# Optimization experiments

Hardware: AMD Instinct MI355X
Metric: run time of the kernel (lower is better)

The kernel has to match this reference:

```python
import jax, jax.numpy as jnp
import numpy as np

B, S, D, E, H, SL = 4, 2048, 2048, 16, 1024, 1
NUM_SLOTS = E * SL
TEMP = 1.0
TOP_K = 2
EPS = 1e-8


def setup_inputs() -> dict:
    key = jax.random.key(0)
    k0, k1, k2, k3 = jax.random.split(key, 4)
    x = jax.random.normal(k0, (B, S, D), dtype=jnp.float32)
    Wd = jax.random.normal(k1, (NUM_SLOTS, D), dtype=jnp.float32) * 0.02
    W1 = jax.random.normal(k2, (E, D, H), dtype=jnp.float32) * 0.02
    b1 = jnp.zeros((E, H), dtype=jnp.float32)
    W2 = jax.random.normal(k3, (E, H, D), dtype=jnp.float32) * 0.02
    b2 = jnp.zeros((E, D), dtype=jnp.float32)
    return {"x": x, "Wd": Wd, "W1": W1, "b1": b1, "W2": W2, "b2": b2}


def reference(x, Wd, W1, b1, W2, b2):
    lead = x.shape[:-1]
    xf = x.reshape(-1, D)                      # [T, D]
    T = xf.shape[0]

    logits = (xf @ Wd.T) / TEMP                # [T, num_slots]
    dispatch = jax.nn.softmax(logits, axis=0)  # softmax over tokens
    combine = jax.nn.softmax(logits, axis=-1)  # softmax over slots

    # Aggregate tokens into slots, run all experts as one batched GEMM chain.
    slot_in = (dispatch.T @ xf).reshape(E, SL, D)                    # [E, SL, D]
    h = jax.nn.gelu(jnp.einsum('esd,edh->esh', slot_in, W1) + b1[:, None, :],
                    approximate=False)
    slot_out = (jnp.einsum('esh,ehd->esd', h, W2) + b2[:, None, :]).reshape(NUM_SLOTS, D)

    out = (combine @ slot_out).reshape(x.shape)

    # Router stats / losses (eval mode: no EMA update of train_scores).
    expert_weights = combine.reshape(T, E, SL).mean(-1)              # [T, E]
    mean_usage = expert_weights.mean(0)                              # [E]
    p = jax.nn.softmax(Wd.mean(0).reshape(E, -1).mean(-1))
    router_loss = E * jnp.sum(mean_usage * p)

    topk_w, topk_idx = jax.lax.top_k(expert_weights, TOP_K)
    topk_w_norm = topk_w / jnp.clip(topk_w.sum(-1, keepdims=True), EPS)

    gate_weights = expert_weights.reshape(*lead, E)
    routing_entropy = -(gate_weights * jnp.log(gate_weights + EPS)).sum(-1).mean()

    return (out,
            router_loss,
            gate_weights,
            topk_idx.reshape(*lead, TOP_K),
            topk_w_norm.reshape(*lead, TOP_K),
            mean_usage,
            routing_entropy,
            dispatch.reshape(*lead, NUM_SLOTS))
```

## Files before the change

kernel.cpp:

```cpp
#include <hip/hip_runtime.h>
#include <math.h>

#define TTOK 8192
#define DIM  2048
#define NEXP 16
#define NH   1024

#define OFF_PART1   0u
#define OFF_LOGITS  2097152u
#define OFF_COMBINE 2228224u
#define OFF_NUM     2359296u
#define OFF_PART6   2490368u
#define OFF_RAWH    4587520u
#define OFF_PART10  4849664u
#define OFF_SLOTOUT 5373952u
#define OFF_CMAX    5406720u
#define OFF_CSUM    5407232u
#define OFF_MUSUM   5407744u
#define OFF_ENT     5408256u
#define OFF_M       5408288u
#define OFF_INVS    5408304u

#define O_OUT   0u
#define O_LOSS  16777216u
#define O_GATE  16777217u
#define O_TOPI  16908289u
#define O_TOPW  16924673u
#define O_MU    16941057u
#define O_ENTR  16941073u
#define O_DISP  16941074u

__device__ __forceinline__ float wave_sum(float v){
  #pragma unroll
  for (int o=1;o<64;o<<=1) v += __shfl_xor(v,o,64);
  return v;
}
__device__ __forceinline__ float wave_max(float v){
  #pragma unroll
  for (int o=1;o<64;o<<=1) v = fmaxf(v,__shfl_xor(v,o,64));
  return v;
}

__global__ __launch_bounds__(256) void k1_logits(const float* __restrict__ x,
                                                 const float* __restrict__ Wd,
                                                 float* __restrict__ part1){
  const int tb = blockIdx.x >> 4;
  const int kc = blockIdx.x & 15;
  const int t  = tb*256 + threadIdx.x;
  const float4* __restrict__ xr = (const float4*)(x + (size_t)t*DIM + kc*128);
  float acc[16];
  #pragma unroll
  for (int e=0;e<16;e++) acc[e]=0.f;
  #pragma unroll 4
  for (int k4=0;k4<32;k4++){
    float4 xv = xr[k4];
    #pragma unroll
    for (int e=0;e<16;e++){
      float4 w = *(const float4*)(Wd + e*DIM + kc*128 + k4*4);
      acc[e] += xv.x*w.x + xv.y*w.y + xv.z*w.z + xv.w*w.w;
    }
  }
  float4* po = (float4*)(part1 + ((size_t)kc*TTOK + t)*16);
  po[0] = make_float4(acc[0],acc[1],acc[2],acc[3]);
  po[1] = make_float4(acc[4],acc[5],acc[6],acc[7]);
  po[2] = make_float4(acc[8],acc[9],acc[10],acc[11]);
  po[3] = make_float4(acc[12],acc[13],acc[14],acc[15]);
}

__global__ __launch_bounds__(256) void k2_row(const float* __restrict__ part1,
    float* __restrict__ logits, float* __restrict__ combine,
    float* __restrict__ gate_out, float* __restrict__ topi_out, float* __restrict__ topw_out,
    float* __restrict__ colmax_part, float* __restrict__ musum_part, float* __restrict__ ent_part){
  const int tid = threadIdx.x;
  const int t = blockIdx.x*256 + tid;
  float l[16];
  #pragma unroll
  for (int e=0;e<16;e++) l[e]=0.f;
  for (int kc=0;kc<16;kc++){
    const float4* pr = (const float4*)(part1 + ((size_t)kc*TTOK + t)*16);
    #pragma unroll
    for (int q=0;q<4;q++){
      float4 v = pr[q];
      l[q*4+0]+=v.x; l[q*4+1]+=v.y; l[q*4+2]+=v.z; l[q*4+3]+=v.w;
    }
  }
  float4* lo = (float4*)(logits + (size_t)t*16);
  lo[0]=make_float4(l[0],l[1],l[2],l[3]);   lo[1]=make_float4(l[4],l[5],l[6],l[7]);
  lo[2]=make_float4(l[8],l[9],l[10],l[11]); lo[3]=make_float4(l[12],l[13],l[14],l[15]);
  float m = l[0];
  #pragma unroll
  for (int e=1;e<16;e++) m = fmaxf(m,l[e]);
  float c[16]; float s=0.f;
  #pragma unroll
  for (int e=0;e<16;e++){ c[e]=expf(l[e]-m); s+=c[e]; }
  float inv = 1.f/s;
  #pragma unroll
  for (int e=0;e<16;e++) c[e]*=inv;
  float4* co = (float4*)(combine + (size_t)t*16);
  co[0]=make_float4(c[0],c[1],c[2],c[3]);   co[1]=make_float4(c[4],c[5],c[6],c[7]);
  co[2]=make_float4(c[8],c[9],c[10],c[11]); co[3]=make_float4(c[12],c[13],c[14],c[15]);
  float* go = gate_out + (size_t)t*16;
  #pragma unroll
  for (int e=0;e<16;e++) go[e]=c[e];
  float v0=-1.f, v1=-1.f; int i0=0, i1=0;
  #pragma unroll
  for (int e=0;e<16;e++){
    float ce=c[e];
    if (ce>v0){ v1=v0; i1=i0; v0=ce; i0=e; }
    else if (ce>v1){ v1=ce; i1=e; }
  }
  float dn = fmaxf(v0+v1, 1e-8f);
  topi_out[(size_t)t*2+0]=(float)i0; topi_out[(size_t)t*2+1]=(float)i1;
  topw_out[(size_t)t*2+0]=v0/dn;     topw_out[(size_t)t*2+1]=v1/dn;
  float ent=0.f;
  #pragma unroll
  for (int e=0;e<16;e++) ent -= c[e]*logf(c[e]+1e-8f);

  __shared__ float red[4][16];
  __shared__ float rede[4];
  const int w = tid>>6, lane = tid&63;
  #pragma unroll
  for (int e=0;e<16;e++){ float v=wave_max(l[e]); if(lane==0) red[w][e]=v; }
  __syncthreads();
  if (tid<16){
    float v=fmaxf(fmaxf(red[0][tid],red[1][tid]),fmaxf(red[2][tid],red[3][tid]));
    colmax_part[blockIdx.x*16+tid]=v;
  }
  __syncthreads();
  #pragma unroll
  for (int e=0;e<16;e++){ float v=wave_sum(c[e]); if(lane==0) red[w][e]=v; }
  { float v=wave_sum(ent); if(lane==0) rede[w]=v; }
  __syncthreads();
  if (tid<16) musum_part[blockIdx.x*16+tid]=red[0][tid]+red[1][tid]+red[2][tid]+red[3][tid];
  if (tid==0) ent_part[blockIdx.x]=rede[0]+rede[1]+rede[2]+rede[3];
}

__global__ __launch_bounds__(256) void k3_finalize(const float* __restrict__ Wd,
    const float* __restrict__ colmax_part, const float* __restrict__ musum_part,
    const float* __restrict__ ent_part,
    float* __restrict__ m_ws, float* __restrict__ loss_out,
    float* __restrict__ mu_out, float* __restrict__ ent_out){
  const int tid = threadIdx.x;
  __shared__ float sq[16][16];
  __shared__ float smu[16];
  __shared__ float sqe[16];
  {
    int s = tid>>4, e = tid&15;
    const float* base = Wd + (size_t)s*DIM + e*128;
    float q=0.f;
    for (int i=0;i<128;i+=4){ float4 v=*(const float4*)(base+i); q+=v.x+v.y+v.z+v.w; }
    sq[s][e]=q;
  }
  if (tid<16){
    float mm=-INFINITY, mu=0.f;
    for (int b=0;b<32;b++){ mm=fmaxf(mm,colmax_part[b*16+tid]); mu+=musum_part[b*16+tid]; }
    m_ws[tid]=mm;
    mu/=8192.f;
    mu_out[tid]=mu; smu[tid]=mu;
  }
  if (tid==32){ float es=0.f; for(int b=0;b<32;b++) es+=ent_part[b]; ent_out[0]=es/8192.f; }
  __syncthreads();
  __shared__ float sqv[16];
  if (tid<16){ float q=0.f; for(int s=0;s<16;s++) q+=sq[s][tid]; sqv[tid]=q/2048.f; }
  __syncthreads();
  if (tid<16){
    float qm=-INFINITY;
    for (int e=0;e<16;e++) qm=fmaxf(qm,sqv[e]);
    sqe[tid]=expf(sqv[tid]-qm);
  }
  __syncthreads();
  if (tid==0){
    float qs=0.f; for(int e=0;e<16;e++) qs+=sqe[e];
    float loss=0.f; for(int e=0;e<16;e++) loss+=smu[e]*(sqe[e]/qs);
    loss_out[0]=16.f*loss;
  }
}

__global__ __launch_bounds__(256) void k4_num(const float* __restrict__ logits,
    const float* __restrict__ m_ws, float* __restrict__ num, float* __restrict__ colsum_part){
  const int tid=threadIdx.x;
  const int t=blockIdx.x*256+tid;
  float mm[16];
  {
    const float4* mp=(const float4*)m_ws;
    #pragma unroll
    for (int q=0;q<4;q++){ float4 v=mp[q]; mm[q*4]=v.x; mm[q*4+1]=v.y; mm[q*4+2]=v.z; mm[q*4+3]=v.w; }
  }
  const float4* lr=(const float4*)(logits+(size_t)t*16);
  float n[16];
  #pragma unroll
  for (int q=0;q<4;q++){
    float4 v=lr[q];
    n[q*4+0]=expf(v.x-mm[q*4+0]); n[q*4+1]=expf(v.y-mm[q*4+1]);
    n[q*4+2]=expf(v.z-mm[q*4+2]); n[q*4+3]=expf(v.w-mm[q*4+3]);
  }
  float4* no=(float4*)(num+(size_t)t*16);
  no[0]=make_float4(n[0],n[1],n[2],n[3]);   no[1]=make_float4(n[4],n[5],n[6],n[7]);
  no[2]=make_float4(n[8],n[9],n[10],n[11]); no[3]=make_float4(n[12],n[13],n[14],n[15]);
  __shared__ float red[4][16];
  const int w=tid>>6, lane=tid&63;
  #pragma unroll
  for (int e=0;e<16;e++){ float v=wave_sum(n[e]); if(lane==0) red[w][e]=v; }
  __syncthreads();
  if (tid<16) colsum_part[blockIdx.x*16+tid]=red[0][tid]+red[1][tid]+red[2][tid]+red[3][tid];
}

__global__ void k5_invs(const float* __restrict__ colsum_part, float* __restrict__ inv_s){
  int tid=threadIdx.x;
  if (tid<16){ float s=0.f; for(int b=0;b<32;b++) s+=colsum_part[b*16+tid]; inv_s[tid]=1.f/s; }
}

__global__ __launch_bounds__(256) void k5b_disp(const float* __restrict__ num,
    const float* __restrict__ inv_s, float* __restrict__ disp_out){
  int i = blockIdx.x*256 + threadIdx.x;
  disp_out[i] = num[i]*inv_s[i&15];
}

__global__ __launch_bounds__(256) void k6_slotin(const float* __restrict__ x,
    const float* __restrict__ num, float* __restrict__ part6){
  const int tc = blockIdx.x >> 2;
  const int dc = blockIdx.x & 3;
  const int d  = dc*512 + threadIdx.x*2;
  const int t0 = tc*128;
  float2 acc[16];
  #pragma unroll
  for (int e=0;e<16;e++){ acc[e].x=0.f; acc[e].y=0.f; }
  #pragma unroll 4
  for (int t=0;t<128;t++){
    float2 xv = *(const float2*)(x + (size_t)(t0+t)*DIM + d);
    const float* nr = num + (size_t)(t0+t)*16;
    #pragma unroll
    for (int e=0;e<16;e++){
      float nv = nr[e];
      acc[e].x = fmaf(nv,xv.x,acc[e].x);
      acc[e].y = fmaf(nv,xv.y,acc[e].y);
    }
  }
  #pragma unroll
  for (int e=0;e<16;e++)
    *(float2*)(part6 + ((size_t)tc*16+e)*DIM + d) = acc[e];
}

__global__ __launch_bounds__(256) void k8_h(const float* __restrict__ part6,
    const float* __restrict__ W1, float* __restrict__ rawh){
  const int e   = blockIdx.x >> 4;
  const int dcc = blockIdx.x & 15;
  const int dbase = dcc*128;
  const int tid = threadIdx.x;
  __shared__ float sl[128];
  if (tid<128){
    float s=0.f;
    for (int tc=0;tc<64;tc++) s += part6[((size_t)tc*16+e)*DIM + dbase + tid];
    sl[tid]=s;
  }
  __syncthreads();
  const int hq = tid*4;
  float4 acc = make_float4(0.f,0.f,0.f,0.f);
  #pragma unroll 8
  for (int d=0; d<128; d++){
    float4 w = *(const float4*)(W1 + ((size_t)e*DIM + dbase + d)*NH + hq);
    float s = sl[d];
    acc.x=fmaf(s,w.x,acc.x); acc.y=fmaf(s,w.y,acc.y);
    acc.z=fmaf(s,w.z,acc.z); acc.w=fmaf(s,w.w,acc.w);
  }
  *(float4*)(rawh + ((size_t)dcc*16+e)*NH + hq) = acc;
}

__global__ __launch_bounds__(256) void k10_so(const float* __restrict__ rawh,
    const float* __restrict__ W2, const float* __restrict__ b1,
    const float* __restrict__ inv_s, float* __restrict__ part10){
  const int e  = blockIdx.x >> 4;
  const int hc = blockIdx.x & 15;
  const int hbase = hc*64;
  const int tid = threadIdx.x;
  __shared__ float hh[64];
  if (tid<64){
    float s=0.f;
    for (int dcc=0;dcc<16;dcc++) s += rawh[((size_t)dcc*16+e)*NH + hbase + tid];
    float pre = inv_s[e]*s + b1[(size_t)e*NH + hbase + tid];
    hh[tid] = 0.5f*pre*(1.f+erff(pre*0.70710678118654752f));
  }
  __syncthreads();
  const int d0 = tid*4, d1 = (tid+256)*4;
  float4 a0=make_float4(0,0,0,0), a1=make_float4(0,0,0,0);
  #pragma unroll 4
  for (int j=0;j<64;j++){
    const float* wrow = W2 + ((size_t)e*NH + hbase + j)*DIM;
    float4 w0 = *(const float4*)(wrow + d0);
    float4 w1 = *(const float4*)(wrow + d1);
    float s = hh[j];
    a0.x=fmaf(s,w0.x,a0.x); a0.y=fmaf(s,w0.y,a0.y); a0.z=fmaf(s,w0.z,a0.z); a0.w=fmaf(s,w0.w,a0.w);
    a1.x=fmaf(s,w1.x,a1.x); a1.y=fmaf(s,w1.y,a1.y); a1.z=fmaf(s,w1.z,a1.z); a1.w=fmaf(s,w1.w,a1.w);
  }
  *(float4*)(part10 + ((size_t)hc*16+e)*DIM + d0) = a0;
  *(float4*)(part10 + ((size_t)hc*16+e)*DIM + d1) = a1;
}

__global__ __launch_bounds__(256) void k11_sofin(const float* __restrict__ part10,
    const float* __restrict__ b2, float* __restrict__ slot_out){
  int i = blockIdx.x*256 + threadIdx.x;
  float s=0.f;
  #pragma unroll
  for (int hc=0;hc<16;hc++) s += part10[(size_t)hc*32768 + i];
  slot_out[i] = s + b2[i];
}

__global__ __launch_bounds__(256) void k12_out(const float* __restrict__ slot_out,
    const float* __restrict__ combine, float* __restrict__ out){
  const int tb = blockIdx.x >> 1;
  const int dc = blockIdx.x & 1;
  const int t0 = tb*32;
  const int d  = dc*1024 + threadIdx.x*4;
  float4 sv[16];
  #pragma unroll
  for (int e=0;e<16;e++) sv[e] = *(const float4*)(slot_out + (size_t)e*DIM + d);
  for (int t=0;t<32;t++){
    const float* cr = combine + (size_t)(t0+t)*16;
    float4 a = make_float4(0,0,0,0);
    #pragma unroll
    for (int e=0;e<16;e++){
      float c = cr[e];
      a.x=fmaf(c,sv[e].x,a.x); a.y=fmaf(c,sv[e].y,a.y);
      a.z=fmaf(c,sv[e].z,a.z); a.w=fmaf(c,sv[e].w,a.w);
    }
    *(float4*)(out + (size_t)(t0+t)*DIM + d) = a;
  }
}

extern "C" void kernel_launch(void* const* d_in, const int* in_sizes, int n_in,
                              void* d_out, int out_size, void* d_ws, size_t ws_size,
                              hipStream_t stream) {
  const float* x  = (const float*)d_in[0];
  const float* Wd = (const float*)d_in[1];
  const float* W1 = (const float*)d_in[2];
  const float* b1 = (const float*)d_in[3];
  const float* W2 = (const float*)d_in[4];
  const float* b2 = (const float*)d_in[5];
  float* out = (float*)d_out;
  float* ws  = (float*)d_ws;

  float* part1   = ws + OFF_PART1;
  float* logits  = ws + OFF_LOGITS;
  float* combine = ws + OFF_COMBINE;
  float* num     = ws + OFF_NUM;
  float* part6   = ws + OFF_PART6;
  float* rawh    = ws + OFF_RAWH;
  float* part10  = ws + OFF_PART10;
  float* slot_out= ws + OFF_SLOTOUT;
  float* cmaxp   = ws + OFF_CMAX;
  float* csump   = ws + OFF_CSUM;
  float* musump  = ws + OFF_MUSUM;
  float* entp    = ws + OFF_ENT;
  float* m_ws    = ws + OFF_M;
  float* inv_s   = ws + OFF_INVS;

  float* o_out  = out + O_OUT;
  float* o_loss = out + O_LOSS;
  float* o_gate = out + O_GATE;
  float* o_topi = out + O_TOPI;
  float* o_topw = out + O_TOPW;
  float* o_mu   = out + O_MU;
  float* o_ent  = out + O_ENTR;
  float* o_disp = out + O_DISP;

  k1_logits<<<512, 256, 0, stream>>>(x, Wd, part1);
  k2_row<<<32, 256, 0, stream>>>(part1, logits, combine, o_gate, o_topi, o_topw,
                                 cmaxp, musump, entp);
  k3_finalize<<<1, 256, 0, stream>>>(Wd, cmaxp, musump, entp, m_ws, o_loss, o_mu, o_ent);
  k4_num<<<32, 256, 0, stream>>>(logits, m_ws, num, csump);
  k5_invs<<<1, 64, 0, stream>>>(csump, inv_s);
  k5b_disp<<<512, 256, 0, stream>>>(num, inv_s, o_disp);
  k6_slotin<<<256, 256, 0, stream>>>(x, num, part6);
  k8_h<<<256, 256, 0, stream>>>(part6, W1, rawh);
  k10_so<<<256, 256, 0, stream>>>(rawh, W2, b1, inv_s, part10);
  k11_sofin<<<128, 256, 0, stream>>>(part10, b2, slot_out);
  k12_out<<<512, 256, 0, stream>>>(slot_out, combine, o_out);
}
```

Measured before the change: 192.7 us.

## Drop column-max pass, split reductions into more blocks across MoE pipeline

Removes the per-column max subtraction from the token-softmax, computing exp(logits) directly and fusing the partial-logit reduction with the column-sum in a new kernel. It also re-tiles the slot aggregation, expert GEMMs and output kernels into many more smaller blocks, with separate reduction and GELU kernels. The aim is to raise occupancy on the small-grid stages and remove one kernel pass. Skipping the max subtraction risks overflow for large logits, and more partial buffers add memory traffic.

New measurement: 199.3 us. +3.4%, slower.

```diff
diff --git a/kernel.cpp b/kernel.cpp
--- a/kernel.cpp
+++ b/kernel.cpp
@@ -3,23 +3,22 @@
 
 #define TTOK 8192
 #define DIM  2048
-#define NEXP 16
 #define NH   1024
 
 #define OFF_PART1   0u
 #define OFF_LOGITS  2097152u
-#define OFF_COMBINE 2228224u
-#define OFF_NUM     2359296u
+#define OFF_NUM     2228224u
+#define OFF_COMBINE 2359296u
 #define OFF_PART6   2490368u
-#define OFF_RAWH    4587520u
-#define OFF_PART10  4849664u
-#define OFF_SLOTOUT 5373952u
-#define OFF_CMAX    5406720u
-#define OFF_CSUM    5407232u
-#define OFF_MUSUM   5407744u
-#define OFF_ENT     5408256u
-#define OFF_M       5408288u
-#define OFF_INVS    5408304u
+#define OFF_SRAW    10878976u
+#define OFF_RAWH    10911744u
+#define OFF_H       11960320u
+#define OFF_PART10  11976704u
+#define OFF_SLOTOUT 14073856u
+#define OFF_CSUM    14106624u
+#define OFF_MUSUM   14108672u
+#define OFF_ENT     14109696u
+#define OFF_INVS    14109760u
 
 #define O_OUT   0u
 #define O_LOSS  16777216u
@@ -33,11 +32,6 @@
 __device__ __forceinline__ float wave_sum(float v){
   #pragma unroll
   for (int o=1;o<64;o<<=1) v += __shfl_xor(v,o,64);
-  return v;
-}
-__device__ __forceinline__ float wave_max(float v){
-  #pragma unroll
-  for (int o=1;o<64;o<<=1) v = fmaxf(v,__shfl_xor(v,o,64));
   return v;
 }
 
@@ -67,26 +61,65 @@
   po[3] = make_float4(acc[12],acc[13],acc[14],acc[15]);
 }
 
-__global__ __launch_bounds__(256) void k2_row(const float* __restrict__ part1,
-    float* __restrict__ logits, float* __restrict__ combine,
-    float* __restrict__ gate_out, float* __restrict__ topi_out, float* __restrict__ topw_out,
-    float* __restrict__ colmax_part, float* __restrict__ musum_part, float* __restrict__ ent_part){
-  const int tid = threadIdx.x;
-  const int t = blockIdx.x*256 + tid;
+__global__ __launch_bounds__(256) void k2a_num(const float* __restrict__ part1,
+    float* __restrict__ logits, float* __restrict__ num, float* __restrict__ colsum_part){
+  const int tid = threadIdx.x;
+  const int i = blockIdx.x*256 + tid;
+  const float4* p1 = (const float4*)part1;
+  float4 s = make_float4(0,0,0,0);
+  #pragma unroll
+  for (int kc=0;kc<16;kc++){
+    float4 v = p1[(size_t)kc*32768 + i];
+    s.x+=v.x; s.y+=v.y; s.z+=v.z; s.w+=v.w;
+  }
+  ((float4*)logits)[i] = s;
+  float4 n = make_float4(expf(s.x),expf(s.y),expf(s.z),expf(s.w));
+  ((float4*)num)[i] = n;
+  #pragma unroll
+  for (int o=4;o<64;o<<=1){
+    n.x += __shfl_xor(n.x,o,64); n.y += __shfl_xor(n.y,o,64);
+    n.z += __shfl_xor(n.z,o,64); n.w += __shfl_xor(n.w,o,64);
+  }
+  __shared__ float4 red[4][4];
+  const int w = tid>>6, lane = tid&63;
+  if (lane<4) red[w][lane] = n;
+  __syncthreads();
+  if (tid<4){
+    float4 a = red[0][tid], b = red[1][tid], c = red[2][tid], d = red[3][tid];
+    float4 t = make_float4(a.x+b.x+c.x+d.x, a.y+b.y+c.y+d.y,
+                           a.z+b.z+c.z+d.z, a.w+b.w+c.w+d.w);
+    *(float4*)(colsum_part + blockIdx.x*16 + tid*4) = t;
+  }
+}
+
+__global__ __launch_bounds__(256) void k5_invs(const float* __restrict__ colsum_part,
+                                               float* __restrict__ inv_s){
+  const int tid = threadIdx.x;
+  const int e = tid&15, sl = tid>>4;
+  float s = 0.f;
+  #pragma unroll
+  for (int k=0;k<8;k++) s += colsum_part[(sl*8+k)*16 + e];
+  __shared__ float L[16][16];
+  L[sl][e] = s;
+  __syncthreads();
+  if (tid<16){
+    float v=0.f;
+    #pragma unroll
+    for (int q=0;q<16;q++) v += L[q][tid];
+    inv_s[tid] = 1.f/v;
+  }
+}
+
+__global__ __launch_bounds__(128) void k2b_row(const float* __restrict__ logits,
+    float* __restrict__ combine, float* __restrict__ gate_out,
+    float* __restrict__ topi_out, float* __restrict__ topw_out,
+    float* __restrict__ musum_part, float* __restrict__ ent_part){
+  const int tid = threadIdx.x;
+  const int t = blockIdx.x*128 + tid;
   float l[16];
-  #pragma unroll
-  for (int e=0;e<16;e++) l[e]=0.f;
-  for (int kc=0;kc<16;kc++){
-    const float4* pr = (const float4*)(part1 + ((size_t)kc*TTOK + t)*16);
-    #pragma unroll
-    for (int q=0;q<4;q++){
-      float4 v = pr[q];
-      l[q*4+0]+=v.x; l[q*4+1]+=v.y; l[q*4+2]+=v.z; l[q*4+3]+=v.w;
-    }
-  }
-  float4* lo = (float4*)(logits + (size_t)t*16);
-  lo[0]=make_float4(l[0],l[1],l[2],l[3]);   lo[1]=make_float4(l[4],l[5],l[6],l[7]);
-  lo[2]=make_float4(l[8],l[9],l[10],l[11]); lo[3]=make_float4(l[12],l[13],l[14],l[15]);
+  const float4* lr = (const float4*)(logits + (size_t)t*16);
+  #pragma unroll
+  for (int q=0;q<4;q++){ float4 v=lr[q]; l[q*4]=v.x; l[q*4+1]=v.y; l[q*4+2]=v.z; l[q*4+3]=v.w; }
   float m = l[0];
   #pragma unroll
   for (int e=1;e<16;e++) m = fmaxf(m,l[e]);
@@ -116,30 +149,20 @@
   #pragma unroll
   for (int e=0;e<16;e++) ent -= c[e]*logf(c[e]+1e-8f);
 
-  __shared__ float red[4][16];
-  __shared__ float rede[4];
+  __shared__ float red[2][16];
+  __shared__ float rede[2];
   const int w = tid>>6, lane = tid&63;
-  #pragma unroll
-  for (int e=0;e<16;e++){ float v=wave_max(l[e]); if(lane==0) red[w][e]=v; }
-  __syncthreads();
-  if (tid<16){
-    float v=fmaxf(fmaxf(red[0][tid],red[1][tid]),fmaxf(red[2][tid],red[3][tid]));
-    colmax_part[blockIdx.x*16+tid]=v;
-  }
-  __syncthreads();
   #pragma unroll
   for (int e=0;e<16;e++){ float v=wave_sum(c[e]); if(lane==0) red[w][e]=v; }
   { float v=wave_sum(ent); if(lane==0) rede[w]=v; }
   __syncthreads();
-  if (tid<16) musum_part[blockIdx.x*16+tid]=red[0][tid]+red[1][tid]+red[2][tid]+red[3][tid];
-  if (tid==0) ent_part[blockIdx.x]=rede[0]+rede[1]+rede[2]+rede[3];
+  if (tid<16) musum_part[blockIdx.x*16+tid]=red[0][tid]+red[1][tid];
+  if (tid==16) ent_part[blockIdx.x]=rede[0]+rede[1];
 }
 
 __global__ __launch_bounds__(256) void k3_finalize(const float* __restrict__ Wd,
-    const float* __restrict__ colmax_part, const float* __restrict__ musum_part,
-    const float* __restrict__ ent_part,
-    float* __restrict__ m_ws, float* __restrict__ loss_out,
-    float* __restrict__ mu_out, float* __restrict__ ent_out){
+    const float* __restrict__ musum_part, const float* __restrict__ ent_part,
+    float* __restrict__ loss_out, float* __restrict__ mu_out, float* __restrict__ ent_out){
   const int tid = threadIdx.x;
   __shared__ float sq[16][16];
   __shared__ float smu[16];
@@ -152,13 +175,12 @@
     sq[s][e]=q;
   }
   if (tid<16){
-    float mm=-INFINITY, mu=0.f;
-    for (int b=0;b<32;b++){ mm=fmaxf(mm,colmax_part[b*16+tid]); mu+=musum_part[b*16+tid]; }
-    m_ws[tid]=mm;
+    float mu=0.f;
+    for (int b=0;b<64;b++) mu += musum_part[b*16+tid];
     mu/=8192.f;
     mu_out[tid]=mu; smu[tid]=mu;
   }
-  if (tid==32){ float es=0.f; for(int b=0;b<32;b++) es+=ent_part[b]; ent_out[0]=es/8192.f; }
+  if (tid==32){ float es=0.f; for(int b=0;b<64;b++) es+=ent_part[b]; ent_out[0]=es/8192.f; }
   __syncthreads();
   __shared__ float sqv[16];
   if (tid<16){ float q=0.f; for(int s=0;s<16;s++) q+=sq[s][tid]; sqv[tid]=q/2048.f; }
@@ -176,40 +198,6 @@
   }
 }
 
-__global__ __launch_bounds__(256) void k4_num(const float* __restrict__ logits,
-    const float* __restrict__ m_ws, float* __restrict__ num, float* __restrict__ colsum_part){
-  const int tid=threadIdx.x;
-  const int t=blockIdx.x*256+tid;
-  float mm[16];
-  {
-    const float4* mp=(const float4*)m_ws;
-    #pragma unroll
-    for (int q=0;q<4;q++){ float4 v=mp[q]; mm[q*4]=v.x; mm[q*4+1]=v.y; mm[q*4+2]=v.z; mm[q*4+3]=v.w; }
-  }
-  const float4* lr=(const float4*)(logits+(size_t)t*16);
-  float n[16];
-  #pragma unroll
-  for (int q=0;q<4;q++){
-    float4 v=lr[q];
-    n[q*4+0]=expf(v.x-mm[q*4+0]); n[q*4+1]=expf(v.y-mm[q*4+1]);
-    n[q*4+2]=expf(v.z-mm[q*4+2]); n[q*4+3]=expf(v.w-mm[q*4+3]);
-  }
-  float4* no=(float4*)(num+(size_t)t*16);
-  no[0]=make_float4(n[0],n[1],n[2],n[3]);   no[1]=make_float4(n[4],n[5],n[6],n[7]);
-  no[2]=make_float4(n[8],n[9],n[10],n[11]); no[3]=make_float4(n[12],n[13],n[14],n[15]);
-  __shared__ float red[4][16];
-  const int w=tid>>6, lane=tid&63;
-  #pragma unroll
-  for (int e=0;e<16;e++){ float v=wave_sum(n[e]); if(lane==0) red[w][e]=v; }
-  __syncthreads();
-  if (tid<16) colsum_part[blockIdx.x*16+tid]=red[0][tid]+red[1][tid]+red[2][tid]+red[3][tid];
-}
-
-__global__ void k5_invs(const float* __restrict__ colsum_part, float* __restrict__ inv_s){
-  int tid=threadIdx.x;
-  if (tid<16){ float s=0.f; for(int b=0;b<32;b++) s+=colsum_part[b*16+tid]; inv_s[tid]=1.f/s; }
-}
-
 __global__ __launch_bounds__(256) void k5b_disp(const float* __restrict__ num,
     const float* __restrict__ inv_s, float* __restrict__ disp_out){
   int i = blockIdx.x*256 + threadIdx.x;
@@ -218,73 +206,96 @@
 
 __global__ __launch_bounds__(256) void k6_slotin(const float* __restrict__ x,
     const float* __restrict__ num, float* __restrict__ part6){
-  const int tc = blockIdx.x >> 2;
-  const int dc = blockIdx.x & 3;
-  const int d  = dc*512 + threadIdx.x*2;
-  const int t0 = tc*128;
-  float2 acc[16];
-  #pragma unroll
-  for (int e=0;e<16;e++){ acc[e].x=0.f; acc[e].y=0.f; }
-  #pragma unroll 4
-  for (int t=0;t<128;t++){
-    float2 xv = *(const float2*)(x + (size_t)(t0+t)*DIM + d);
-    const float* nr = num + (size_t)(t0+t)*16;
+  const int tc = blockIdx.x >> 1;
+  const int dc = blockIdx.x & 1;
+  const int d  = dc*1024 + threadIdx.x*4;
+  const int t0 = tc*32;
+  __shared__ float4 sN[128];
+  if (threadIdx.x < 128) sN[threadIdx.x] = ((const float4*)num)[t0*4 + threadIdx.x];
+  __syncthreads();
+  float4 acc[16];
+  #pragma unroll
+  for (int e=0;e<16;e++) acc[e]=make_float4(0,0,0,0);
+  #pragma unroll 2
+  for (int t=0;t<32;t++){
+    const float4 xv = *(const float4*)(x + (size_t)(t0+t)*DIM + d);
     #pragma unroll
-    for (int e=0;e<16;e++){
-      float nv = nr[e];
-      acc[e].x = fmaf(nv,xv.x,acc[e].x);
-      acc[e].y = fmaf(nv,xv.y,acc[e].y);
+    for (int q=0;q<4;q++){
+      float4 nq = sN[t*4+q];
+      acc[q*4+0].x=fmaf(nq.x,xv.x,acc[q*4+0].x); acc[q*4+0].y=fmaf(nq.x,xv.y,acc[q*4+0].y);
+      acc[q*4+0].z=fmaf(nq.x,xv.z,acc[q*4+0].z); acc[q*4+0].w=fmaf(nq.x,xv.w,acc[q*4+0].w);
+      acc[q*4+1].x=fmaf(nq.y,xv.x,acc[q*4+1].x); acc[q*4+1].y=fmaf(nq.y,xv.y,acc[q*4+1].y);
+      acc[q*4+1].z=fmaf(nq.y,xv.z,acc[q*4+1].z); acc[q*4+1].w=fmaf(nq.y,xv.w,acc[q*4+1].w);
+      acc[q*4+2].x=fmaf(nq.z,xv.x,acc[q*4+2].x); acc[q*4+2].y=fmaf(nq.z,xv.y,acc[q*4+2].y);
+      acc[q*4+2].z=fmaf(nq.z,xv.z,acc[q*4+2].z); acc[q*4+2].w=fmaf(nq.z,xv.w,acc[q*4+2].w);
+      acc[q*4+3].x=fmaf(nq.w,xv.x,acc[q*4+3].x); acc[q*4+3].y=fmaf(nq.w,xv.y,acc[q*4+3].y);
+      acc[q*4+3].z=fmaf(nq.w,xv.z,acc[q*4+3].z); acc[q*4+3].w=fmaf(nq.w,xv.w,acc[q*4+3].w);
     }
   }
   #pragma unroll
   for (int e=0;e<16;e++)
-    *(float2*)(part6 + ((size_t)tc*16+e)*DIM + d) = acc[e];
-}
-
-__global__ __launch_bounds__(256) void k8_h(const float* __restrict__ part6,
+    *(float4*)(part6 + ((size_t)tc*16+e)*DIM + d) = acc[e];
+}
+
+__global__ __launch_bounds__(256) void k7_sraw(const float* __restrict__ part6,
+    const float* __restrict__ inv_s, float* __restrict__ slot_raw){
+  const int tid = threadIdx.x;
+  const int half = tid>>7, il = tid&127;
+  const int i = blockIdx.x*128 + il;
+  float s=0.f;
+  #pragma unroll 8
+  for (int tc=half*128; tc<half*128+128; tc++) s += part6[(size_t)tc*32768 + i];
+  __shared__ float s2[256];
+  s2[tid]=s;
+  __syncthreads();
+  if (tid<128){
+    int ii = blockIdx.x*128 + tid;
+    slot_raw[ii] = inv_s[ii>>11]*(s2[tid]+s2[tid+128]);
+  }
+}
+
+__global__ __launch_bounds__(256) void k8_h(const float* __restrict__ slot_raw,
     const float* __restrict__ W1, float* __restrict__ rawh){
-  const int e   = blockIdx.x >> 4;
-  const int dcc = blockIdx.x & 15;
-  const int dbase = dcc*128;
-  const int tid = threadIdx.x;
-  __shared__ float sl[128];
-  if (tid<128){
-    float s=0.f;
-    for (int tc=0;tc<64;tc++) s += part6[((size_t)tc*16+e)*DIM + dbase + tid];
-    sl[tid]=s;
-  }
-  __syncthreads();
-  const int hq = tid*4;
-  float4 acc = make_float4(0.f,0.f,0.f,0.f);
-  #pragma unroll 8
-  for (int d=0; d<128; d++){
+  const int e  = blockIdx.x >> 6;
+  const int dc = blockIdx.x & 63;
+  const int dbase = dc*32;
+  float sl[32];
+  #pragma unroll
+  for (int d=0;d<32;d++) sl[d] = slot_raw[e*DIM + dbase + d];
+  const int hq = threadIdx.x*4;
+  float4 acc = make_float4(0,0,0,0);
+  #pragma unroll
+  for (int d=0;d<32;d++){
     float4 w = *(const float4*)(W1 + ((size_t)e*DIM + dbase + d)*NH + hq);
     float s = sl[d];
     acc.x=fmaf(s,w.x,acc.x); acc.y=fmaf(s,w.y,acc.y);
     acc.z=fmaf(s,w.z,acc.z); acc.w=fmaf(s,w.w,acc.w);
   }
-  *(float4*)(rawh + ((size_t)dcc*16+e)*NH + hq) = acc;
-}
-
-__global__ __launch_bounds__(256) void k10_so(const float* __restrict__ rawh,
-    const float* __restrict__ W2, const float* __restrict__ b1,
-    const float* __restrict__ inv_s, float* __restrict__ part10){
-  const int e  = blockIdx.x >> 4;
-  const int hc = blockIdx.x & 15;
-  const int hbase = hc*64;
-  const int tid = threadIdx.x;
-  __shared__ float hh[64];
-  if (tid<64){
-    float s=0.f;
-    for (int dcc=0;dcc<16;dcc++) s += rawh[((size_t)dcc*16+e)*NH + hbase + tid];
-    float pre = inv_s[e]*s + b1[(size_t)e*NH + hbase + tid];
-    hh[tid] = 0.5f*pre*(1.f+erff(pre*0.70710678118654752f));
-  }
-  __syncthreads();
-  const int d0 = tid*4, d1 = (tid+256)*4;
+  *(float4*)(rawh + ((size_t)dc*16+e)*NH + hq) = acc;
+}
+
+__global__ __launch_bounds__(256) void k9_gelu(const float* __restrict__ rawh,
+    const float* __restrict__ b1, float* __restrict__ hbuf){
+  const int i = blockIdx.x*256 + threadIdx.x;
+  float s=0.f;
+  #pragma unroll 8
+  for (int dc=0;dc<64;dc++) s += rawh[(size_t)dc*16384 + i];
+  float pre = s + b1[i];
+  hbuf[i] = 0.5f*pre*(1.f+erff(pre*0.70710678118654752f));
+}
+
+__global__ __launch_bounds__(256) void k10_so(const float* __restrict__ hbuf,
+    const float* __restrict__ W2, float* __restrict__ part10){
+  const int e  = blockIdx.x >> 6;
+  const int hc = blockIdx.x & 63;
+  const int hbase = hc*16;
+  float hh[16];
+  #pragma unroll
+  for (int j=0;j<16;j++) hh[j] = hbuf[e*NH + hbase + j];
+  const int d0 = threadIdx.x*4, d1 = d0 + 1024;
   float4 a0=make_float4(0,0,0,0), a1=make_float4(0,0,0,0);
-  #pragma unroll 4
-  for (int j=0;j<64;j++){
+  #pragma unroll
+  for (int j=0;j<16;j++){
     const float* wrow = W2 + ((size_t)e*NH + hbase + j)*DIM;
     float4 w0 = *(const float4*)(wrow + d0);
     float4 w1 = *(const float4*)(wrow + d1);
@@ -298,23 +309,32 @@
 
 __global__ __launch_bounds__(256) void k11_sofin(const float* __restrict__ part10,
     const float* __restrict__ b2, float* __restrict__ slot_out){
-  int i = blockIdx.x*256 + threadIdx.x;
+  const int tid = threadIdx.x;
+  const int half = tid>>7, il = tid&127;
+  const int i = blockIdx.x*128 + il;
   float s=0.f;
-  #pragma unroll
-  for (int hc=0;hc<16;hc++) s += part10[(size_t)hc*32768 + i];
-  slot_out[i] = s + b2[i];
+  #pragma unroll 8
+  for (int hc=half*32; hc<half*32+32; hc++) s += part10[(size_t)hc*32768 + i];
+  __shared__ float s2[256];
+  s2[tid]=s;
+  __syncthreads();
+  if (tid<128){
+    int ii = blockIdx.x*128 + tid;
+    slot_out[ii] = s2[tid]+s2[tid+128] + b2[ii];
+  }
 }
 
 __global__ __launch_bounds__(256) void k12_out(const float* __restrict__ slot_out,
     const float* __restrict__ combine, float* __restrict__ out){
   const int tb = blockIdx.x >> 1;
   const int dc = blockIdx.x & 1;
-  const int t0 = tb*32;
+  const int t0 = tb*16;
   const int d  = dc*1024 + threadIdx.x*4;
   float4 sv[16];
   #pragma unroll
   for (int e=0;e<16;e++) sv[e] = *(const float4*)(slot_out + (size_t)e*DIM + d);
-  for (int t=0;t<32;t++){
+  #pragma unroll 2
+  for (int t=0;t<16;t++){
     const float* cr = combine + (size_t)(t0+t)*16;
     float4 a = make_float4(0,0,0,0);
     #pragma unroll
@@ -341,38 +361,31 @@
 
   float* part1   = ws + OFF_PART1;
   float* logits  = ws + OFF_LOGITS;
+  float* num     = ws + OFF_NUM;
   float* combine = ws + OFF_COMBINE;
-  float* num     = ws + OFF_NUM;
   float* part6   = ws + OFF_PART6;
+  float* sraw    = ws + OFF_SRAW;
   float* rawh    = ws + OFF_RAWH;
+  float* hbuf    = ws + OFF_H;
   float* part10  = ws + OFF_PART10;
   float* slot_out= ws + OFF_SLOTOUT;
-  float* cmaxp   = ws + OFF_CMAX;
   float* csump   = ws + OFF_CSUM;
   float* musump  = ws + OFF_MUSUM;
   float* entp    = ws + OFF_ENT;
-  float* m_ws    = ws + OFF_M;
   float* inv_s   = ws + OFF_INVS;
 
-  float* o_out  = out + O_OUT;
-  float* o_loss = out + O_LOSS;
-  float* o_gate = out + O_GATE;
-  float* o_topi = out + O_TOPI;
-  float* o_topw = out + O_TOPW;
-  float* o_mu   = out + O_MU;
-  float* o_ent  = out + O_ENTR;
-  float* o_disp = out + O_DISP;
-
   k1_logits<<<512, 256, 0, stream>>>(x, Wd, part1);
-  k2_row<<<32, 256, 0, stream>>>(part1, logits, combine, o_gate, o_topi, o_topw,
-                                 cmaxp, musump, entp);
-  k3_finalize<<<1, 256, 0, stream>>>(Wd, cmaxp, musump, entp, m_ws, o_loss, o_mu, o_ent);
-  k4_num<<<32, 256, 0, stream>>>(logits, m_ws, num, csump);
-  k5_invs<<<1, 64, 0, stream>>>(csump, inv_s);
-  k5b_disp<<<512, 256, 0, stream>>>(num, inv_s, o_disp);
-  k6_slotin<<<256, 256, 0, stream>>>(x, num, part6);
-  k8_h<<<256, 256, 0, stream>>>(part6, W1, rawh);
-  k10_so<<<256, 256, 0, stream>>>(rawh, W2, b1, inv_s, part10);
-  k11_sofin<<<128, 256, 0, stream>>>(part10, b2, slot_out);
-  k12_out<<<512, 256, 0, stream>>>(slot_out, combine, o_out);
-}
+  k2a_num<<<128, 256, 0, stream>>>(part1, logits, num, csump);
+  k5_invs<<<1, 256, 0, stream>>>(csump, inv_s);
+  k2b_row<<<64, 128, 0, stream>>>(logits, combine, out + O_GATE, out + O_TOPI,
+                                  out + O_TOPW, musump, entp);
+  k3_finalize<<<1, 256, 0, stream>>>(Wd, musump, entp, out + O_LOSS, out + O_MU, out + O_ENTR);
+  k5b_disp<<<512, 256, 0, stream>>>(num, inv_s, out + O_DISP);
+  k6_slotin<<<512, 256, 0, stream>>>(x, num, part6);
+  k7_sraw<<<256, 256, 0, stream>>>(part6, inv_s, sraw);
+  k8_h<<<1024, 256, 0, stream>>>(sraw, W1, rawh);
+  k9_gelu<<<64, 256, 0, stream>>>(rawh, b1, hbuf);
+  k10_so<<<1024, 256, 0, stream>>>(hbuf, W2, part10);
+  k11_sofin<<<256, 256, 0, stream>>>(part10, b2, slot_out);
+  k12_out<<<1024, 256, 0, stream>>>(slot_out, combine, out + O_OUT);
+}
```
